# Kernel optimization log

Hardware: AMD Instinct MI355X
Metric: run time of the kernel (lower is better)

Reference implementation:

```python
import jax, jax.numpy as jnp
import numpy as np

N = 4096
DIM = 128      # dim_in
HID = 256      # mlp hidden_dim
K_IN = 8       # k for linear_k

def _knn_edges(dist, k):
    # dist: [n,n]; k nearest neighbors excluding self (matches heapq loop)
    n = dist.shape[0]
    d = jnp.where(jnp.eye(n, dtype=bool), jnp.inf, dist)
    nbr = jax.lax.top_k(-d, k)[1]                     # [n,k] indices of k smallest
    src = jnp.repeat(jnp.arange(n), k)                # res[0] = i
    dst = nbr.reshape(-1)                             # res[1] = neighbor
    return src, dst

def _gcn_conv(x, src, dst, W, b):
    # torch_geometric GCNConv: add self loops + symmetric normalization
    n = x.shape[0]
    loop = jnp.arange(n)
    s = jnp.concatenate([src, loop])
    t = jnp.concatenate([dst, loop])
    xw = x @ W
    deg = jax.ops.segment_sum(jnp.ones(s.shape[0], x.dtype), t, num_segments=n)
    dinv = jax.lax.rsqrt(deg)                         # deg >= 1 due to self loops
    norm = dinv[s] * dinv[t]
    out = jax.ops.segment_sum(norm[:, None] * xw[s], t, num_segments=n)
    return out + b

def _gcn(x, src, dst, Wg1, bg1, Wg2, bg2):
    h = jax.nn.relu(_gcn_conv(x, src, dst, Wg1, bg1))
    h = _gcn_conv(h, src, dst, Wg2, bg2)              # dropout is identity in eval
    return jax.nn.log_softmax(h, axis=1)

def _conv2d(x, w, b):
    y = jax.lax.conv_general_dilated(x, w, (1, 1), 'SAME',
        dimension_numbers=('NCHW', 'OIHW', 'NCHW'))
    return y + b.reshape(1, -1, 1, 1)

def setup_inputs():
    key = jax.random.key(0)
    ks = jax.random.split(key, 20)
    f32 = jnp.float32
    def w(k, shape):
        fan = shape[0]
        return (jax.random.uniform(k, shape, f32) * 2 - 1) * (1.0 / np.sqrt(fan))
    return {
        'data_x_1': jax.random.normal(ks[0], (1, N, 4), f32),
        'data_x_2': jax.random.normal(ks[1], (1, N, K_IN, 4), f32),
        'Wk': w(ks[2], (K_IN, 1)),        'bk': jnp.zeros((1,), f32),
        'Wg1': w(ks[3], (8, DIM // 2)),   'bg1': jnp.zeros((DIM // 2,), f32),
        'Wg2': w(ks[4], (DIM // 2, DIM)), 'bg2': jnp.zeros((DIM,), f32),
        'Wq': w(ks[5], (3 * DIM, DIM)),   'bq': jnp.zeros((DIM,), f32),
        'Wkey': w(ks[6], (3 * DIM, DIM)), 'bkey': jnp.zeros((DIM,), f32),
        'Woff': w(ks[7], (4, DIM)),       'boff': jnp.zeros((DIM,), f32),
        'pw': jnp.full((1,), 0.25, f32),
        'Wf1': w(ks[8], (DIM, HID)),      'bf1': jnp.zeros((HID,), f32),
        'Wf2': w(ks[9], (HID, HID)),      'bf2': jnp.zeros((HID,), f32),
        'Wf3': w(ks[10], (HID, 4)),       'bf3': jnp.zeros((4,), f32),
        'Wcy3': w(ks[11], (1, 1, 1, 3)),  'bcy3': jnp.zeros((1,), f32),
        'Wcx3': w(ks[12], (1, 1, 3, 1)),  'bcx3': jnp.zeros((1,), f32),
        'Wcy5': w(ks[13], (1, 1, 1, 5)),  'bcy5': jnp.zeros((1,), f32),
        'Wcx5': w(ks[14], (1, 1, 5, 1)),  'bcx5': jnp.zeros((1,), f32),
        'Wcy9': w(ks[15], (1, 1, 1, 9)),  'bcy9': jnp.zeros((1,), f32),
        'Wcx9': w(ks[16], (1, 1, 9, 1)),  'bcx9': jnp.zeros((1,), f32),
    }

def reference(data_x_1, data_x_2, Wk, bk, Wg1, bg1, Wg2, bg2, Wq, bq, Wkey, bkey,
              Woff, boff, pw, Wf1, bf1, Wf2, bf2, Wf3, bf3,
              Wcy3, bcy3, Wcx3, bcx3, Wcy5, bcy5, Wcx5, bcx5, Wcy9, bcy9, Wcx9, bcx9):
    # linear_k over k dimension: [1,n,k,4] -> transpose -> [1,n,4,k] -> [1,n,4]
    dx2 = jnp.swapaxes(data_x_2, 2, 3)
    dx2_out = (dx2 @ Wk + bk)[..., 0]
    data_x = jnp.concatenate([data_x_1, dx2_out], axis=2)   # [1,n,8]
    Ot = data_x[:, :, 4:]                                   # [1,n,4]

    pos = data_x[:, :, 0:2]
    diff = pos[:, :, None, :] - pos[:, None, :, :]          # [1,n,n,2]
    distances = jnp.linalg.norm(diff, axis=3)               # [1,n,n]
    maxd = jnp.max(distances, axis=2, keepdims=True)
    oushi_atte = 1.0 - distances / maxd                     # [1,n,n]

    x0 = data_x[0]
    dist0 = jax.lax.stop_gradient(distances[0])             # knn on detached dist
    embs = []
    for kk in (3, 5, 9):
        src, dst = _knn_edges(dist0, kk)
        embs.append(_gcn(x0, src, dst, Wg1, bg1, Wg2, bg2)[None])
    embedding = jnp.concatenate(embs, axis=2)               # [1,n,3*DIM]

    query = embedding @ Wq + bq                             # [1,n,DIM]
    key_t = embedding @ Wkey + bkey
    scores = jnp.einsum('bnd,bmd->bnm', query, key_t) / jnp.sqrt(jnp.float32(DIM))
    A = scores / jnp.max(scores, axis=2, keepdims=True)     # [1,n,n]

    A4 = A[None]                                            # [1,1,n,n]
    c3 = _conv2d(A4, Wcy3, bcy3) + _conv2d(A4, Wcx3, bcx3)
    c5 = _conv2d(A4, Wcy5, bcy5) + _conv2d(A4, Wcx5, bcx5)
    c9 = _conv2d(A4, Wcy9, bcy9) + _conv2d(A4, Wcx9, bcx9)

    A_cat = jnp.concatenate([A, oushi_atte, c3[0], c5[0], c9[0]], axis=2)  # [1,n,5n]
    A_cat = (A_cat - A_cat.min()) / (A_cat.max() - A_cat.min())

    Ot5 = jnp.tile(Ot, (1, 5, 1))                           # [1,5n,4]
    h = jnp.matmul(A_cat, Ot5)                              # [1,n,4]
    h = h @ Woff + boff                                     # [1,n,DIM]
    h = jnp.where(h > 0, h, pw * h)                         # PReLU (scalar weight)
    h = jax.nn.relu(h @ Wf1 + bf1)
    h = jax.nn.relu(h @ Wf2 + bf2)
    return h @ Wf3 + bf3                                    # [1,n,4]
```

## Files before the change

kernel.cpp:

```cpp
#include <hip/hip_runtime.h>
#include <math.h>

#define NN 4096

typedef __bf16 bf16x8 __attribute__((ext_vector_type(8)));
typedef float  f32x4  __attribute__((ext_vector_type(4)));

static __device__ __forceinline__ unsigned enc_f(float f){
    unsigned u = __float_as_uint(f);
    return (u & 0x80000000u) ? ~u : (u | 0x80000000u);
}
static __device__ __forceinline__ float dec_f(unsigned u){
    unsigned b = (u & 0x80000000u) ? (u & 0x7fffffffu) : ~u;
    return __uint_as_float(b);
}
static __device__ __forceinline__ float4 shfl4(float4 v, int src){
    float4 r;
    r.x = __shfl(v.x, src, 64);
    r.y = __shfl(v.y, src, 64);
    r.z = __shfl(v.z, src, 64);
    r.w = __shfl(v.w, src, 64);
    return r;
}

__global__ void k_prep(const float* __restrict__ dx1, const float* __restrict__ dx2,
                       const float* __restrict__ Wk, const float* __restrict__ bk,
                       float* __restrict__ x0, float* __restrict__ colsum){
    int n = blockIdx.x*blockDim.x + threadIdx.x;
    if (n >= NN) return;
    float wk[8];
    #pragma unroll
    for (int j=0;j<8;j++) wk[j] = Wk[j];
    float bkv = bk[0];
    #pragma unroll
    for (int c=0;c<4;c++) x0[n*8+c] = dx1[n*4+c];
    #pragma unroll
    for (int c=0;c<4;c++){
        float acc = bkv;
        #pragma unroll
        for (int j=0;j<8;j++) acc += dx2[(n*8+j)*4+c]*wk[j];
        x0[n*8+4+c] = acc;
        atomicAdd(&colsum[c], acc);
    }
}

__global__ void k_ty(const float* __restrict__ x0,
        const float* __restrict__ Wcy3, const float* __restrict__ Wcy5, const float* __restrict__ Wcy9,
        float* __restrict__ Ty){
    int j = blockIdx.x*256 + threadIdx.x;
    if (j >= NN) return;
    float Cy[9];
    #pragma unroll
    for (int o=-4;o<=4;o++){
        float c = Wcy9[o+4];
        if (o>=-2 && o<=2) c += Wcy5[o+2];
        if (o>=-1 && o<=1) c += Wcy3[o+1];
        Cy[o+4] = c;
    }
    float4 acc = {0,0,0,0};
    #pragma unroll
    for (int o=-4;o<=4;o++){
        int jj = j - o;
        if ((unsigned)jj < NN){
            float4 ot = *(const float4*)&x0[jj*8+4];
            float c = Cy[o+4];
            acc.x += c*ot.x; acc.y += c*ot.y; acc.z += c*ot.z; acc.w += c*ot.w;
        }
    }
    *(float4*)&Ty[j*4] = acc;
}

__global__ __launch_bounds__(256) void k_dist(const float* __restrict__ dx1,
        const float* __restrict__ x0,
        float* __restrict__ maxd, int* __restrict__ nbr,
        int* __restrict__ cnt3, int* __restrict__ cnt5, int* __restrict__ cnt9,
        float* __restrict__ dOt){
    __shared__ float2 ps[NN];
    int tid = threadIdx.x;
    for (int j=tid; j<NN; j+=256){
        float4 v = *(const float4*)&dx1[j*4];
        ps[j] = make_float2(v.x, v.y);
    }
    __syncthreads();
    int lane = tid & 63;
    int i = blockIdx.x*4 + (tid>>6);
    float2 pi = ps[i];
    unsigned long long best[9];
    #pragma unroll
    for (int q=0;q<9;q++) best[q] = ~0ULL;
    float lmax = 0.f;
    float4 dacc = {0,0,0,0};
    for (int t=0;t<64;t++){
        int j = (t<<6) | lane;
        float2 p = ps[j];
        float dx = pi.x - p.x, dy = pi.y - p.y;
        float d = sqrtf(dx*dx + dy*dy);
        lmax = fmaxf(lmax, d);
        float4 otj = *(const float4*)&x0[j*8+4];
        dacc.x += d*otj.x; dacc.y += d*otj.y; dacc.z += d*otj.z; dacc.w += d*otj.w;
        unsigned long long cand = ((unsigned long long)__float_as_uint(d) << 32) | (unsigned)j;
        if (j != i && cand < best[8]){
            best[8] = cand;
            #pragma unroll
            for (int q=8; q>0; --q){
                if (best[q] < best[q-1]){ unsigned long long tm=best[q]; best[q]=best[q-1]; best[q-1]=tm; }
            }
        }
    }
    #pragma unroll
    for (int m=1;m<64;m<<=1){
        lmax = fmaxf(lmax, __shfl_xor(lmax, m, 64));
        dacc.x += __shfl_xor(dacc.x, m, 64);
        dacc.y += __shfl_xor(dacc.y, m, 64);
        dacc.z += __shfl_xor(dacc.z, m, 64);
        dacc.w += __shfl_xor(dacc.w, m, 64);
    }
    if (lane==0){
        maxd[i] = lmax;
        *(float4*)&dOt[i*4] = dacc;
    }
    for (int t=0;t<9;t++){
        unsigned long long w = best[0];
        #pragma unroll
        for (int m=1;m<64;m<<=1){
            unsigned long long o = __shfl_xor(w, m, 64);
            if (o < w) w = o;
        }
        if (best[0] == w){
            #pragma unroll
            for (int q=0;q<8;q++) best[q] = best[q+1];
            best[8] = ~0ULL;
        }
        if (lane==0){
            int j = (int)(w & 0xffffffffu);
            nbr[i*9+t] = j;
            atomicAdd(&cnt9[j], 1);
            if (t<5) atomicAdd(&cnt5[j], 1);
            if (t<3) atomicAdd(&cnt3[j], 1);
        }
    }
}

__global__ __launch_bounds__(256) void k_scan(const int* __restrict__ cnt3,
        const int* __restrict__ cnt5, const int* __restrict__ cnt9,
        int* __restrict__ offc, float* __restrict__ dinvc){
    __shared__ int part[256];
    int tid = threadIdx.x;
    for (int g=0; g<3; g++){
        const int* cp = g==0?cnt3:(g==1?cnt5:cnt9);
        int base = tid*16;
        int loc[16]; int s=0;
        #pragma unroll
        for (int q=0;q<16;q++){ loc[q]=s; s += cp[base+q]; }
        part[tid]=s; __syncthreads();
        for (int d=1; d<256; d<<=1){
            int v = (tid>=d) ? part[tid-d] : 0;
            __syncthreads();
            part[tid] += v;
            __syncthreads();
        }
        int pre = (tid==0) ? 0 : part[tid-1];
        #pragma unroll
        for (int q=0;q<16;q++){
            offc[g*NN + base + q]  = pre + loc[q];
            dinvc[g*NN + base + q] = rsqrtf((float)cp[base+q] + 1.f);
        }
        __syncthreads();
    }
}

__global__ void k_fill(const int* __restrict__ nbr, const int* __restrict__ offc,
        int* __restrict__ cur, int* __restrict__ rev){
    int i = blockIdx.x*256 + threadIdx.x;
    if (i >= NN) return;
    #pragma unroll
    for (int t=0;t<9;t++){
        int j = nbr[i*9+t];
        int gmin = t<3 ? 0 : (t<5 ? 1 : 2);
        for (int g=gmin; g<3; g++){
            int pos = atomicAdd(&cur[g*NN+j], 1);
            int rb = (g==0) ? 0 : (g==1 ? NN*3 : NN*8);
            rev[rb + offc[g*NN+j] + pos] = i;
        }
    }
}

__global__ void k_y1(const float* __restrict__ x0, const float* __restrict__ Wg1,
                     float* __restrict__ xw){
    int idx = blockIdx.x*256 + threadIdx.x;
    if (idx >= NN*64) return;
    int n = idx>>6, c = idx&63;
    float acc = 0.f;
    #pragma unroll
    for (int k=0;k<8;k++) acc += x0[n*8+k]*Wg1[k*64+c];
    xw[idx] = acc;
}

__global__ __launch_bounds__(256) void k_h1y2(const float* __restrict__ xw,
        const int* __restrict__ offc,
        const int* __restrict__ cnt3, const int* __restrict__ cnt5, const int* __restrict__ cnt9,
        const int* __restrict__ rev, const float* __restrict__ dinvc,
        const float* __restrict__ bg1, const float* __restrict__ Wg2,
        float* __restrict__ y2){
    __shared__ float h1s[12][64];
    int n0 = blockIdx.x*4, tid = threadIdx.x;
    for (int s=tid; s<768; s+=256){
        int p = s>>6, k = s&63, g = p>>2, n = n0+(p&3);
        const int* cp = g==0?cnt3:(g==1?cnt5:cnt9);
        int rb = (g==0) ? 0 : (g==1 ? NN*3 : NN*8);
        int cnt = cp[n];
        int o = rb + offc[g*NN+n];
        float dv = dinvc[g*NN+n];
        float srow = dv*xw[n*64+k];
        for (int e=0;e<cnt;e++){
            int i = rev[o+e];
            srow += dinvc[g*NN+i]*xw[i*64+k];
        }
        float v = dv*srow + bg1[k];
        h1s[p][k] = v>0.f ? v : 0.f;
    }
    __syncthreads();
    int c = tid & 127, ph = tid>>7;
    float a6[6] = {0,0,0,0,0,0};
    for (int k=0;k<64;k++){
        float w = Wg2[k*128+c];
        #pragma unroll
        for (int q=0;q<6;q++) a6[q] += h1s[q*2+ph][k]*w;
    }
    #pragma unroll
    for (int q=0;q<6;q++){
        int p = q*2+ph, g = p>>2, n = n0+(p&3);
        float dv = dinvc[g*NN+n];
        y2[(size_t)g*NN*128 + (size_t)n*128 + c] = dv*a6[q];
    }
}

__global__ __launch_bounds__(128) void k_fin(const float* __restrict__ y2,
        const int* __restrict__ offc,
        const int* __restrict__ cnt3, const int* __restrict__ cnt5, const int* __restrict__ cnt9,
        const int* __restrict__ rev, const float* __restrict__ dinvc,
        const float* __restrict__ bg2, float* __restrict__ emb){
    __shared__ float sm[2], ss[2];
    int b = blockIdx.x;
    int n = b & (NN-1), g = b >> 12;
    const int* cp = g==0?cnt3:(g==1?cnt5:cnt9);
    int rb = (g==0) ? 0 : (g==1 ? NN*3 : NN*8);
    int cnt = cp[n];
    int o = rb + offc[g*NN+n];
    float dv = dinvc[g*NN+n];
    int c = threadIdx.x;
    const float* yg = y2 + (size_t)g*NN*128;
    float s = yg[(size_t)n*128 + c];
    for (int e=0;e<cnt;e++){
        int i = rev[o+e];
        s += yg[(size_t)i*128 + c];
    }
    float v = dv*s + bg2[c];
    float m = v;
    #pragma unroll
    for (int st=1;st<64;st<<=1) m = fmaxf(m, __shfl_xor(m, st, 64));
    if ((c&63)==0) sm[c>>6] = m;
    __syncthreads();
    m = fmaxf(sm[0], sm[1]);
    float e = expf(v - m);
    float t = e;
    #pragma unroll
    for (int st=1;st<64;st<<=1) t += __shfl_xor(t, st, 64);
    if ((c&63)==0) ss[c>>6] = t;
    __syncthreads();
    t = ss[0]+ss[1];
    emb[n*384 + g*128 + c] = v - m - logf(t);
}

__global__ __launch_bounds__(256) void k_qk(const float* __restrict__ emb,
        const float* __restrict__ Wq, const float* __restrict__ bq,
        const float* __restrict__ Wkey, const float* __restrict__ bkey,
        __bf16* __restrict__ qh, __bf16* __restrict__ ql,
        __bf16* __restrict__ kh, __bf16* __restrict__ kl){
    __shared__ float es[8][384];
    int n0 = blockIdx.x*8;
    int tid = threadIdx.x;
    for (int idx=tid; idx<8*384; idx+=256){
        int m = idx/384, k = idx%384;
        es[m][k] = emb[(n0+m)*384+k];
    }
    __syncthreads();
    int c = tid & 127;
    int sel = tid >> 7;
    const float* W = sel ? Wkey : Wq;
    float b = sel ? bkey[c] : bq[c];
    float acc[8];
    #pragma unroll
    for (int m=0;m<8;m++) acc[m]=b;
    for (int k=0;k<384;k++){
        float w = W[k*128+c];
        #pragma unroll
        for (int m=0;m<8;m++) acc[m] += es[m][k]*w;
    }
    __bf16* oh = sel ? kh : qh;
    __bf16* ol = sel ? kl : ql;
    #pragma unroll
    for (int m=0;m<8;m++){
        float v = acc[m];
        __bf16 h = (__bf16)v;
        oh[(size_t)(n0+m)*128+c] = h;
        ol[(size_t)(n0+m)*128+c] = (__bf16)(v - (float)h);
    }
}

__global__ __launch_bounds__(256) void k_scores(
        const __bf16* __restrict__ qh, const __bf16* __restrict__ ql,
        const __bf16* __restrict__ kh, const __bf16* __restrict__ kl,
        float* __restrict__ scores,
        unsigned* __restrict__ rowmaxenc, unsigned* __restrict__ rowminenc){
    int bx = blockIdx.x & 31;
    int by = blockIdx.x >> 5;
    int tid = threadIdx.x;
    int w = tid >> 6, lane = tid & 63;
    int li = lane & 15, g = lane >> 4;
    int r0 = by*128 + (w>>1)*64;
    int c0 = bx*128 + (w&1)*64;

    f32x4 acc[4][4] = {};
    for (int ks=0; ks<4; ++ks){
        int kofs = ks*32 + g*8;
        bf16x8 ah[4], al[4], bh[4], bl[4];
        #pragma unroll
        for (int f=0; f<4; ++f){
            ah[f] = *(const bf16x8*)&qh[(size_t)(r0+f*16+li)*128 + kofs];
            al[f] = *(const bf16x8*)&ql[(size_t)(r0+f*16+li)*128 + kofs];
            bh[f] = *(const bf16x8*)&kh[(size_t)(c0+f*16+li)*128 + kofs];
            bl[f] = *(const bf16x8*)&kl[(size_t)(c0+f*16+li)*128 + kofs];
        }
        #pragma unroll
        for (int fr=0; fr<4; ++fr){
            #pragma unroll
            for (int fc=0; fc<4; ++fc){
                acc[fr][fc] = __builtin_amdgcn_mfma_f32_16x16x32_bf16(ah[fr], bh[fc], acc[fr][fc], 0, 0, 0);
                acc[fr][fc] = __builtin_amdgcn_mfma_f32_16x16x32_bf16(ah[fr], bl[fc], acc[fr][fc], 0, 0, 0);
                acc[fr][fc] = __builtin_amdgcn_mfma_f32_16x16x32_bf16(al[fr], bh[fc], acc[fr][fc], 0, 0, 0);
            }
        }
    }
    #pragma unroll
    for (int fr=0; fr<4; ++fr){
        #pragma unroll
        for (int r=0; r<4; ++r){
            int row = r0 + fr*16 + g*4 + r;
            float mx = -INFINITY, mn = INFINITY;
            #pragma unroll
            for (int fc=0; fc<4; ++fc){
                float v = acc[fr][fc][r];
                scores[(size_t)row*NN + c0 + fc*16 + li] = v;
                mx = fmaxf(mx, v);
                mn = fminf(mn, v);
            }
            #pragma unroll
            for (int s=1; s<16; s<<=1){
                mx = fmaxf(mx, __shfl_xor(mx, s, 64));
                mn = fminf(mn, __shfl_xor(mn, s, 64));
            }
            if (li == 0){
                atomicMax(&rowmaxenc[row], enc_f(mx));
                atomicMin(&rowminenc[row], enc_f(mn));
            }
        }
    }
}

__global__ void k_invr(const unsigned* __restrict__ rowmaxenc, float* __restrict__ invr){
    int i = blockIdx.x*256 + threadIdx.x;
    if (i >= NN) return;
    invr[i] = 1.f/dec_f(rowmaxenc[i]);
}

__global__ __launch_bounds__(256) void k_cfuse(const float* __restrict__ scores,
        const float* __restrict__ invr,
        const float* __restrict__ x0, const float* __restrict__ Ty,
        const float* __restrict__ Wcy3, const float* __restrict__ Wcx3,
        const float* __restrict__ Wcy5, const float* __restrict__ Wcx5,
        const float* __restrict__ Wcy9, const float* __restrict__ Wcx9,
        const float* __restrict__ bcy3, const float* __restrict__ bcx3,
        const float* __restrict__ bcy5, const float* __restrict__ bcx5,
        const float* __restrict__ bcy9, const float* __restrict__ bcx9,
        float* __restrict__ mnmx, float* __restrict__ hpart){
    __shared__ float smn[4], smx[4];
    int tid = threadIdx.x;
    int w = tid >> 6, lane = tid & 63;
    int strip = blockIdx.x;
    int rb = blockIdx.y*4 + w;
    int i0 = rb*28;
    int colbase = strip*248 - 4 + lane*4;
    bool lv = (colbase >= 0) && (colbase + 3 < NN);
    bool outLane = (lane >= 1) && (lane < 63) && lv;

    float wy3[3],wx3[3],wy5[5],wx5[5],wy9[9],wx9[9];
    #pragma unroll
    for (int t=0;t<3;t++){ wy3[t]=Wcy3[t]; wx3[t]=Wcx3[t]; }
    #pragma unroll
    for (int t=0;t<5;t++){ wy5[t]=Wcy5[t]; wx5[t]=Wcx5[t]; }
    #pragma unroll
    for (int t=0;t<9;t++){ wy9[t]=Wcy9[t]; wx9[t]=Wcx9[t]; }
    float bc3 = bcy3[0]+bcx3[0];
    float bc5 = bcy5[0]+bcx5[0];
    float bc9 = bcy9[0]+bcx9[0];

    float4 ot[4], ty[4];
    #pragma unroll
    for (int c=0;c<4;c++){
        if (lv){
            ot[c] = *(const float4*)&x0[(colbase+c)*8+4];
            ty[c] = *(const float4*)&Ty[(colbase+c)*4];
        } else {
            ot[c] = make_float4(0,0,0,0);
            ty[c] = make_float4(0,0,0,0);
        }
    }

    float4 win[9];
    float mn = INFINITY, mx = -INFINITY;
    const int laneL = lane - 1, laneR = lane + 1;

    for (int tb = 0; tb < 4; ++tb){
        #pragma unroll
        for (int u = 0; u < 9; ++u){
            int t  = tb*9 + u;
            int ri = i0 - 4 + t;
            float4 a = make_float4(0,0,0,0);
            if (((unsigned)ri < NN) && lv){
                float iv = invr[ri];
                float4 v = *(const float4*)&scores[(size_t)ri*NN + colbase];
                a.x = v.x*iv; a.y = v.y*iv; a.z = v.z*iv; a.w = v.w*iv;
            }
            win[u] = a;
            int ro = i0 + t - 8;
            if (t >= 8 && ro < NN){
                float4 ctr = win[(u+5)%9];
                float4 wl = shfl4(ctr, laneL);
                float4 wr = shfl4(ctr, laneR);
                float cw[12] = {wl.x,wl.y,wl.z,wl.w, ctr.x,ctr.y,ctr.z,ctr.w, wr.x,wr.y,wr.z,wr.w};
                float4 pA = make_float4(0,0,0,0), pT = make_float4(0,0,0,0);
                if (outLane){
                    #pragma unroll
                    for (int c=0;c<4;c++){
                        float cx9 = ((win[(u+1)%9][c]*wx9[0] + win[(u+2)%9][c]*wx9[1]) + (win[(u+3)%9][c]*wx9[2] + win[(u+4)%9][c]*wx9[3]))
                                  + ((win[(u+5)%9][c]*wx9[4] + win[(u+6)%9][c]*wx9[5]) + (win[(u+7)%9][c]*wx9[6] + win[(u+8)%9][c]*wx9[7]))
                                  + win[u][c]*wx9[8];
                        float cx5 = ((win[(u+3)%9][c]*wx5[0] + win[(u+4)%9][c]*wx5[1]) + (win[(u+5)%9][c]*wx5[2] + win[(u+6)%9][c]*wx5[3]))
                                  + win[(u+7)%9][c]*wx5[4];
                        float cx3 = (win[(u+4)%9][c]*wx3[0] + win[(u+5)%9][c]*wx3[1]) + win[(u+6)%9][c]*wx3[2];
                        float cy9 = ((cw[c+0]*wy9[0] + cw[c+1]*wy9[1]) + (cw[c+2]*wy9[2] + cw[c+3]*wy9[3]))
                                  + ((cw[c+4]*wy9[4] + cw[c+5]*wy9[5]) + (cw[c+6]*wy9[6] + cw[c+7]*wy9[7]))
                                  + cw[c+8]*wy9[8];
                        float cy5 = ((cw[c+2]*wy5[0] + cw[c+3]*wy5[1]) + (cw[c+4]*wy5[2] + cw[c+5]*wy5[3]))
                                  + cw[c+6]*wy5[4];
                        float cy3 = (cw[c+3]*wy3[0] + cw[c+4]*wy3[1]) + cw[c+5]*wy3[2];
                        float c3v = cy3+cx3+bc3, c5v = cy5+cx5+bc5, c9v = cy9+cx9+bc9;
                        mn = fminf(mn, fminf(fminf(c3v,c5v),c9v));
                        mx = fmaxf(mx, fmaxf(fmaxf(c3v,c5v),c9v));
                        float av = cw[c+4];
                        pA.x += av*ot[c].x; pA.y += av*ot[c].y; pA.z += av*ot[c].z; pA.w += av*ot[c].w;
                        pT.x += av*ty[c].x; pT.y += av*ty[c].y; pT.z += av*ty[c].z; pT.w += av*ty[c].w;
                    }
                }
                #pragma unroll
                for (int m=1; m<64; m<<=1){
                    pA.x += __shfl_xor(pA.x, m, 64); pA.y += __shfl_xor(pA.y, m, 64);
                    pA.z += __shfl_xor(pA.z, m, 64); pA.w += __shfl_xor(pA.w, m, 64);
                    pT.x += __shfl_xor(pT.x, m, 64); pT.y += __shfl_xor(pT.y, m, 64);
                    pT.z += __shfl_xor(pT.z, m, 64); pT.w += __shfl_xor(pT.w, m, 64);
                }
                if (lane == 0){
                    float* hp = &hpart[((size_t)ro*17 + strip)*8];
                    *(float4*)hp = pA;
                    *(float4*)(hp+4) = pT;
                }
            }
        }
    }
    #pragma unroll
    for (int m=1; m<64; m<<=1){
        mn = fminf(mn, __shfl_xor(mn, m, 64));
        mx = fmaxf(mx, __shfl_xor(mx, m, 64));
    }
    if (lane == 0){ smn[w] = mn; smx[w] = mx; }
    __syncthreads();
    if (tid == 0){
        float a0 = fminf(fminf(smn[0],smn[1]), fminf(smn[2],smn[3]));
        float b0 = fmaxf(fmaxf(smx[0],smx[1]), fmaxf(smx[2],smx[3]));
        int bid = blockIdx.y*gridDim.x + blockIdx.x;
        mnmx[bid] = a0;
        mnmx[640 + bid] = b0;
    }
}

__global__ __launch_bounds__(256) void k_gmm(const float* __restrict__ mnmx,
        const unsigned* __restrict__ rowminenc, const unsigned* __restrict__ rowmaxenc,
        float* __restrict__ gmm){
    __shared__ float smn[256], smx[256];
    int tid = threadIdx.x;
    float mn = 0.f, mx = 1.f;
    for (int i=tid; i<NN; i+=256){
        float rmx = dec_f(rowmaxenc[i]);
        float q = dec_f(rowminenc[i]) / rmx;
        mn = fminf(mn, fminf(1.f, q));
        mx = fmaxf(mx, fmaxf(1.f, q));
    }
    for (int b=tid; b<629; b+=256){
        mn = fminf(mn, mnmx[b]);
        mx = fmaxf(mx, mnmx[640+b]);
    }
    smn[tid]=mn; smx[tid]=mx; __syncthreads();
    for (int s=128;s>0;s>>=1){
        if (tid<s){ smn[tid]=fminf(smn[tid],smn[tid+s]); smx[tid]=fmaxf(smx[tid],smx[tid+s]); }
        __syncthreads();
    }
    if (tid==0){ gmm[0]=smn[0]; gmm[1]=smx[0]; }
}

__global__ void k_hred(const float* __restrict__ hpart,
        const float* __restrict__ maxd, const float* __restrict__ dOt,
        const float* __restrict__ colsum,
        const float* __restrict__ bcy3, const float* __restrict__ bcx3,
        const float* __restrict__ bcy5, const float* __restrict__ bcx5,
        const float* __restrict__ bcy9, const float* __restrict__ bcx9,
        float* __restrict__ ASdot, float* __restrict__ Bv){
    int i = blockIdx.x*256 + threadIdx.x;
    if (i >= NN) return;
    float4 pa = {0,0,0,0}, pt = {0,0,0,0};
    const float* hp = &hpart[(size_t)i*17*8];
    #pragma unroll
    for (int s=0; s<17; ++s){
        float4 a = *(const float4*)&hp[s*8];
        float4 t = *(const float4*)&hp[s*8+4];
        pa.x+=a.x; pa.y+=a.y; pa.z+=a.z; pa.w+=a.w;
        pt.x+=t.x; pt.y+=t.y; pt.z+=t.z; pt.w+=t.w;
    }
    float imv = 1.f/maxd[i];
    float bcsum = bcy3[0]+bcx3[0]+bcy5[0]+bcx5[0]+bcy9[0]+bcx9[0];
    float k = 1.f + bcsum;
    float4 cs = *(const float4*)colsum;
    float4 dv = *(const float4*)&dOt[i*4];
    float4 b;
    b.x = cs.x*k - imv*dv.x + pt.x;
    b.y = cs.y*k - imv*dv.y + pt.y;
    b.z = cs.z*k - imv*dv.z + pt.z;
    b.w = cs.w*k - imv*dv.w + pt.w;
    *(float4*)&ASdot[i*4] = pa;
    *(float4*)&Bv[i*4]    = b;
}

__global__ void k_hfin(const float* __restrict__ ASdot, const float* __restrict__ Bv,
        const float* __restrict__ Wcx3, const float* __restrict__ Wcx5, const float* __restrict__ Wcx9,
        const float* __restrict__ gmm, const float* __restrict__ colsum,
        float* __restrict__ hfin){
    int i = blockIdx.x*256 + threadIdx.x;
    if (i >= NN) return;
    float Cx[9];
    #pragma unroll
    for (int o=-4;o<=4;o++){
        float c = Wcx9[o+4];
        if (o>=-2 && o<=2) c += Wcx5[o+2];
        if (o>=-1 && o<=1) c += Wcx3[o+1];
        Cx[o+4] = c;
    }
    float4 h = *(const float4*)&Bv[i*4];
    float4 a0 = *(const float4*)&ASdot[i*4];
    h.x += a0.x; h.y += a0.y; h.z += a0.z; h.w += a0.w;
    #pragma unroll
    for (int o=-4;o<=4;o++){
        int r = i + o;
        if ((unsigned)r < NN){
            float4 av = *(const float4*)&ASdot[r*4];
            float c = Cx[o+4];
            h.x += c*av.x; h.y += c*av.y; h.z += c*av.z; h.w += c*av.w;
        }
    }
    float mnv = gmm[0], mxv = gmm[1];
    float s = 1.f/(mxv-mnv), oa = -mnv*s;
    float4 cs = *(const float4*)colsum;
    float4 out;
    out.x = s*h.x + 5.f*oa*cs.x;
    out.y = s*h.y + 5.f*oa*cs.y;
    out.z = s*h.z + 5.f*oa*cs.z;
    out.w = s*h.w + 5.f*oa*cs.w;
    *(float4*)&hfin[i*4] = out;
}

__global__ __launch_bounds__(256) void k_mlp(const float* __restrict__ hfin,
        const float* __restrict__ Woff, const float* __restrict__ boff, const float* __restrict__ pw,
        const float* __restrict__ Wf1, const float* __restrict__ bf1,
        const float* __restrict__ Wf2, const float* __restrict__ bf2,
        const float* __restrict__ Wf3, const float* __restrict__ bf3,
        float* __restrict__ out){
    __shared__ float h1[8][128];
    __shared__ float h2[8][256];
    __shared__ float h3[8][256];
    __shared__ float4 red4[256];
    int n0 = blockIdx.x*8, tid = threadIdx.x;
    float p = pw[0];
    {
        int c = tid & 127, mb = (tid>>7)*4;
        #pragma unroll
        for (int mm=0; mm<4; mm++){
            int m = mb+mm;
            float v = boff[c];
            #pragma unroll
            for (int k=0;k<4;k++) v += hfin[(n0+m)*4+k]*Woff[k*128+c];
            h1[m][c] = v>0.f ? v : p*v;
        }
    }
    __syncthreads();
    {
        int c = tid;
        float acc[8];
        #pragma unroll
        for (int m=0;m<8;m++) acc[m] = bf1[c];
        for (int k=0;k<128;k++){
            float w = Wf1[k*256+c];
            #pragma unroll
            for (int m=0;m<8;m++) acc[m] += h1[m][k]*w;
        }
        #pragma unroll
        for (int m=0;m<8;m++) h2[m][c] = acc[m]>0.f?acc[m]:0.f;
    }
    __syncthreads();
    {
        int c = tid;
        float acc[8];
        #pragma unroll
        for (int m=0;m<8;m++) acc[m] = bf2[c];
        for (int k=0;k<256;k++){
            float w = Wf2[k*256+c];
            #pragma unroll
            for (int m=0;m<8;m++) acc[m] += h2[m][k]*w;
        }
        #pragma unroll
        for (int m=0;m<8;m++) h3[m][c] = acc[m]>0.f?acc[m]:0.f;
    }
    __syncthreads();
    float w3_0 = Wf3[tid*4+0], w3_1 = Wf3[tid*4+1], w3_2 = Wf3[tid*4+2], w3_3 = Wf3[tid*4+3];
    for (int m=0;m<8;m++){
        float hv = h3[m][tid];
        float4 r; r.x = hv*w3_0; r.y = hv*w3_1; r.z = hv*w3_2; r.w = hv*w3_3;
        red4[tid]=r; __syncthreads();
        for (int s=128;s>0;s>>=1){
            if(tid<s){
                red4[tid].x+=red4[tid+s].x; red4[tid].y+=red4[tid+s].y;
                red4[tid].z+=red4[tid+s].z; red4[tid].w+=red4[tid+s].w;
            }
            __syncthreads();
        }
        if (tid==0){
            float4 o;
            o.x = red4[0].x + bf3[0]; o.y = red4[0].y + bf3[1];
            o.z = red4[0].z + bf3[2]; o.w = red4[0].w + bf3[3];
            *(float4*)&out[(n0+m)*4] = o;
        }
        __syncthreads();
    }
}

extern "C" void kernel_launch(void* const* d_in, const int* in_sizes, int n_in,
                              void* d_out, int out_size, void* d_ws, size_t ws_size,
                              hipStream_t stream){
    const float* dx1  = (const float*)d_in[0];
    const float* dx2  = (const float*)d_in[1];
    const float* Wk   = (const float*)d_in[2];
    const float* bk   = (const float*)d_in[3];
    const float* Wg1  = (const float*)d_in[4];
    const float* bg1  = (const float*)d_in[5];
    const float* Wg2  = (const float*)d_in[6];
    const float* bg2  = (const float*)d_in[7];
    const float* Wq   = (const float*)d_in[8];
    const float* bq   = (const float*)d_in[9];
    const float* Wkey = (const float*)d_in[10];
    const float* bkey = (const float*)d_in[11];
    const float* Woff = (const float*)d_in[12];
    const float* boff = (const float*)d_in[13];
    const float* pw   = (const float*)d_in[14];
    const float* Wf1  = (const float*)d_in[15];
    const float* bf1  = (const float*)d_in[16];
    const float* Wf2  = (const float*)d_in[17];
    const float* bf2  = (const float*)d_in[18];
    const float* Wf3  = (const float*)d_in[19];
    const float* bf3  = (const float*)d_in[20];
    const float* Wcy3 = (const float*)d_in[21];
    const float* bcy3 = (const float*)d_in[22];
    const float* Wcx3 = (const float*)d_in[23];
    const float* bcx3 = (const float*)d_in[24];
    const float* Wcy5 = (const float*)d_in[25];
    const float* bcy5 = (const float*)d_in[26];
    const float* Wcx5 = (const float*)d_in[27];
    const float* bcx5 = (const float*)d_in[28];
    const float* Wcy9 = (const float*)d_in[29];
    const float* bcy9 = (const float*)d_in[30];
    const float* Wcx9 = (const float*)d_in[31];
    const float* bcx9 = (const float*)d_in[32];

    char* ws = (char*)d_ws;
    size_t off = 0;
    auto alloc = [&](size_t b)->void*{ void* p = ws + off; off += (b + 255) & ~(size_t)255; return p; };

    char* zbase = ws + off;
    float*    colsum    = (float*)   alloc(4*4);
    int*      cnt3      = (int*)     alloc((size_t)NN*4);
    int*      cnt5      = (int*)     alloc((size_t)NN*4);
    int*      cnt9      = (int*)     alloc((size_t)NN*4);
    int*      cur       = (int*)     alloc((size_t)3*NN*4);
    unsigned* rowmaxenc = (unsigned*)alloc((size_t)NN*4);
    size_t zbytes = (size_t)((ws + off) - zbase);
    unsigned* rowminenc = (unsigned*)alloc((size_t)NN*4);

    float* x0     = (float*)alloc((size_t)NN*8*4);
    float* maxd   = (float*)alloc((size_t)NN*4);
    int*   nbr    = (int*)  alloc((size_t)NN*9*4);
    int*   offc   = (int*)  alloc((size_t)3*NN*4);
    float* dinvc  = (float*)alloc((size_t)3*NN*4);
    int*   rev    = (int*)  alloc((size_t)NN*17*4);
    float* xw     = (float*)alloc((size_t)NN*64*4);
    float* y2     = (float*)alloc((size_t)3*NN*128*4);
    float* emb    = (float*)alloc((size_t)NN*384*4);
    __bf16* qh   = (__bf16*)alloc((size_t)NN*128*2);
    __bf16* ql   = (__bf16*)alloc((size_t)NN*128*2);
    __bf16* kh   = (__bf16*)alloc((size_t)NN*128*2);
    __bf16* kl   = (__bf16*)alloc((size_t)NN*128*2);
    float* scores = (float*)alloc((size_t)NN*NN*4);
    float* Tyb    = (float*)alloc((size_t)NN*4*4);
    float* invr   = (float*)alloc((size_t)NN*4);
    float* dOt    = (float*)alloc((size_t)NN*4*4);
    float* ASd    = (float*)alloc((size_t)NN*4*4);
    float* Bv     = (float*)alloc((size_t)NN*4*4);
    float* hpart  = (float*)alloc((size_t)NN*17*8*4);
    float* mnmx   = (float*)alloc((size_t)2*640*4);
    float* gmm    = (float*)alloc(2*4);
    float* hfin   = (float*)alloc((size_t)NN*4*4);
    (void)ws_size; (void)in_sizes; (void)n_in; (void)out_size;

    hipMemsetAsync(zbase, 0, zbytes, stream);
    hipMemsetAsync(rowminenc, 0xFF, (size_t)NN*4, stream);

    k_prep<<<16,256,0,stream>>>(dx1,dx2,Wk,bk,x0,colsum);
    k_ty  <<<16,256,0,stream>>>(x0,Wcy3,Wcy5,Wcy9,Tyb);
    k_dist<<<NN/4,256,0,stream>>>(dx1,x0,maxd,nbr,cnt3,cnt5,cnt9,dOt);
    k_scan<<<1,256,0,stream>>>(cnt3,cnt5,cnt9,offc,dinvc);
    k_fill<<<16,256,0,stream>>>(nbr,offc,cur,rev);

    k_y1  <<<NN*64/256,256,0,stream>>>(x0,Wg1,xw);
    k_h1y2<<<NN/4,256,0,stream>>>(xw,offc,cnt3,cnt5,cnt9,rev,dinvc,bg1,Wg2,y2);
    k_fin <<<NN*3,128,0,stream>>>(y2,offc,cnt3,cnt5,cnt9,rev,dinvc,bg2,emb);

    k_qk<<<NN/8,256,0,stream>>>(emb,Wq,bq,Wkey,bkey,qh,ql,kh,kl);
    k_scores<<<1024,256,0,stream>>>(qh,ql,kh,kl,scores,rowmaxenc,rowminenc);
    k_invr<<<16,256,0,stream>>>(rowmaxenc,invr);

    k_cfuse<<<dim3(17,37),256,0,stream>>>(scores,invr,x0,Tyb,
        Wcy3,Wcx3,Wcy5,Wcx5,Wcy9,Wcx9,
        bcy3,bcx3,bcy5,bcx5,bcy9,bcx9, mnmx, hpart);
    k_gmm<<<1,256,0,stream>>>(mnmx,rowminenc,rowmaxenc,gmm);
    k_hred<<<16,256,0,stream>>>(hpart,maxd,dOt,colsum,
        bcy3,bcx3,bcy5,bcx5,bcy9,bcx9, ASd, Bv);
    k_hfin<<<16,256,0,stream>>>(ASd,Bv,Wcx3,Wcx5,Wcx9,gmm,colsum,hfin);
    k_mlp<<<NN/8,256,0,stream>>>(hfin,Woff,boff,pw,Wf1,bf1,Wf2,bf2,Wf3,bf3,(float*)d_out);
}
```

Measured before the change: 334.5 us.

## Compute A·Ot and A·Ty via associativity q·(Kᵀ·Ot) instead of inside conv pass

```diff
diff --git a/kernel.cpp b/kernel.cpp
--- a/kernel.cpp
+++ b/kernel.cpp
@@ -374,22 +374,20 @@
     invr[i] = 1.f/dec_f(rowmaxenc[i]);
 }
 
-__global__ __launch_bounds__(256) void k_cfuse(const float* __restrict__ scores,
+__global__ __launch_bounds__(256) void k_cconv(const float* __restrict__ scores,
         const float* __restrict__ invr,
-        const float* __restrict__ x0, const float* __restrict__ Ty,
         const float* __restrict__ Wcy3, const float* __restrict__ Wcx3,
         const float* __restrict__ Wcy5, const float* __restrict__ Wcx5,
         const float* __restrict__ Wcy9, const float* __restrict__ Wcx9,
         const float* __restrict__ bcy3, const float* __restrict__ bcx3,
         const float* __restrict__ bcy5, const float* __restrict__ bcx5,
         const float* __restrict__ bcy9, const float* __restrict__ bcx9,
-        float* __restrict__ mnmx, float* __restrict__ hpart){
+        float* __restrict__ mnmx){
     __shared__ float smn[4], smx[4];
     int tid = threadIdx.x;
     int w = tid >> 6, lane = tid & 63;
     int strip = blockIdx.x;
-    int rb = blockIdx.y*4 + w;
-    int i0 = rb*28;
+    int i0 = (blockIdx.y*4 + w)*19;
     int colbase = strip*248 - 4 + lane*4;
     bool lv = (colbase >= 0) && (colbase + 3 < NN);
     bool outLane = (lane >= 1) && (lane < 63) && lv;
@@ -405,23 +403,11 @@
     float bc5 = bcy5[0]+bcx5[0];
     float bc9 = bcy9[0]+bcx9[0];
 
-    float4 ot[4], ty[4];
-    #pragma unroll
-    for (int c=0;c<4;c++){
-        if (lv){
-            ot[c] = *(const float4*)&x0[(colbase+c)*8+4];
-            ty[c] = *(const float4*)&Ty[(colbase+c)*4];
-        } else {
-            ot[c] = make_float4(0,0,0,0);
-            ty[c] = make_float4(0,0,0,0);
-        }
-    }
-
     float4 win[9];
     float mn = INFINITY, mx = -INFINITY;
     const int laneL = lane - 1, laneR = lane + 1;
 
-    for (int tb = 0; tb < 4; ++tb){
+    for (int tb = 0; tb < 3; ++tb){
         #pragma unroll
         for (int u = 0; u < 9; ++u){
             int t  = tb*9 + u;
@@ -438,9 +424,8 @@
                 float4 ctr = win[(u+5)%9];
                 float4 wl = shfl4(ctr, laneL);
                 float4 wr = shfl4(ctr, laneR);
-                float cw[12] = {wl.x,wl.y,wl.z,wl.w, ctr.x,ctr.y,ctr.z,ctr.w, wr.x,wr.y,wr.z,wr.w};
-                float4 pA = make_float4(0,0,0,0), pT = make_float4(0,0,0,0);
                 if (outLane){
+                    float cw[12] = {wl.x,wl.y,wl.z,wl.w, ctr.x,ctr.y,ctr.z,ctr.w, wr.x,wr.y,wr.z,wr.w};
                     #pragma unroll
                     for (int c=0;c<4;c++){
                         float cx9 = ((win[(u+1)%9][c]*wx9[0] + win[(u+2)%9][c]*wx9[1]) + (win[(u+3)%9][c]*wx9[2] + win[(u+4)%9][c]*wx9[3]))
@@ -458,22 +443,7 @@
                         float c3v = cy3+cx3+bc3, c5v = cy5+cx5+bc5, c9v = cy9+cx9+bc9;
                         mn = fminf(mn, fminf(fminf(c3v,c5v),c9v));
                         mx = fmaxf(mx, fmaxf(fmaxf(c3v,c5v),c9v));
-                        float av = cw[c+4];
-                        pA.x += av*ot[c].x; pA.y += av*ot[c].y; pA.z += av*ot[c].z; pA.w += av*ot[c].w;
-                        pT.x += av*ty[c].x; pT.y += av*ty[c].y; pT.z += av*ty[c].z; pT.w += av*ty[c].w;
                     }
-                }
-                #pragma unroll
-                for (int m=1; m<64; m<<=1){
-                    pA.x += __shfl_xor(pA.x, m, 64); pA.y += __shfl_xor(pA.y, m, 64);
-                    pA.z += __shfl_xor(pA.z, m, 64); pA.w += __shfl_xor(pA.w, m, 64);
-                    pT.x += __shfl_xor(pT.x, m, 64); pT.y += __shfl_xor(pT.y, m, 64);
-                    pT.z += __shfl_xor(pT.z, m, 64); pT.w += __shfl_xor(pT.w, m, 64);
-                }
-                if (lane == 0){
-                    float* hp = &hpart[((size_t)ro*17 + strip)*8];
-                    *(float4*)hp = pA;
-                    *(float4*)(hp+4) = pT;
                 }
             }
         }
@@ -490,7 +460,79 @@
         float b0 = fmaxf(fmaxf(smx[0],smx[1]), fmaxf(smx[2],smx[3]));
         int bid = blockIdx.y*gridDim.x + blockIdx.x;
         mnmx[bid] = a0;
-        mnmx[640 + bid] = b0;
+        mnmx[1024 + bid] = b0;
+    }
+}
+
+__global__ __launch_bounds__(256) void k_kot(const __bf16* __restrict__ kh, const __bf16* __restrict__ kl,
+        const float* __restrict__ x0, const float* __restrict__ Ty,
+        float* __restrict__ kOt){
+    __shared__ float red[256][8];
+    int d = blockIdx.x, tid = threadIdx.x;
+    float a[8] = {0,0,0,0,0,0,0,0};
+    for (int j = tid; j < NN; j += 256){
+        float kv = (float)kh[(size_t)j*128 + d] + (float)kl[(size_t)j*128 + d];
+        float4 ot = *(const float4*)&x0[j*8+4];
+        float4 ty = *(const float4*)&Ty[j*4];
+        a[0] += kv*ot.x; a[1] += kv*ot.y; a[2] += kv*ot.z; a[3] += kv*ot.w;
+        a[4] += kv*ty.x; a[5] += kv*ty.y; a[6] += kv*ty.z; a[7] += kv*ty.w;
+    }
+    #pragma unroll
+    for (int q=0;q<8;q++) red[tid][q] = a[q];
+    __syncthreads();
+    for (int s=128; s>0; s>>=1){
+        if (tid < s){
+            #pragma unroll
+            for (int q=0;q<8;q++) red[tid][q] += red[tid+s][q];
+        }
+        __syncthreads();
+    }
+    if (tid < 8) kOt[d*8 + tid] = red[0][tid];
+}
+
+__global__ __launch_bounds__(256) void k_asd(
+        const __bf16* __restrict__ qh, const __bf16* __restrict__ ql,
+        const float* __restrict__ kOt,
+        const unsigned* __restrict__ rowmaxenc, const float* __restrict__ maxd,
+        const float* __restrict__ dOt, const float* __restrict__ colsum,
+        const float* __restrict__ bcy3, const float* __restrict__ bcx3,
+        const float* __restrict__ bcy5, const float* __restrict__ bcx5,
+        const float* __restrict__ bcy9, const float* __restrict__ bcx9,
+        float* __restrict__ ASdot, float* __restrict__ Bv){
+    __shared__ float kst[128*8];
+    int tid = threadIdx.x;
+    for (int s = tid; s < 1024; s += 256) kst[s] = kOt[s];
+    __syncthreads();
+    int lane = tid & 63, r = tid >> 6;
+    int i = blockIdx.x*4 + r;
+    float a[8] = {0,0,0,0,0,0,0,0};
+    #pragma unroll
+    for (int dd=0; dd<2; ++dd){
+        int d = lane + dd*64;
+        float qv = (float)qh[(size_t)i*128 + d] + (float)ql[(size_t)i*128 + d];
+        #pragma unroll
+        for (int q=0;q<8;q++) a[q] += qv * kst[d*8+q];
+    }
+    #pragma unroll
+    for (int m=1; m<64; m<<=1){
+        #pragma unroll
+        for (int q=0;q<8;q++) a[q] += __shfl_xor(a[q], m, 64);
+    }
+    if (lane == 0){
+        float iv = 1.f/dec_f(rowmaxenc[i]);
+        float imv = 1.f/maxd[i];
+        float bcsum = bcy3[0]+bcx3[0]+bcy5[0]+bcx5[0]+bcy9[0]+bcx9[0];
+        float k = 1.f + bcsum;
+        float4 cs = *(const float4*)colsum;
+        float4 dv = *(const float4*)&dOt[i*4];
+        float4 pa = {iv*a[0], iv*a[1], iv*a[2], iv*a[3]};
+        float4 b;
+        b.x = cs.x*k - imv*dv.x + iv*a[4];
+        b.y = cs.y*k - imv*dv.y + iv*a[5];
+        b.z = cs.z*k - imv*dv.z + iv*a[6];
+        b.w = cs.w*k - imv*dv.w + iv*a[7];
+        *(float4*)&ASdot[i*4] = pa;
+        *(float4*)&Bv[i*4]    = b;
     }
 }
 
@@ -506,9 +548,9 @@
         mn = fminf(mn, fminf(1.f, q));
         mx = fmaxf(mx, fmaxf(1.f, q));
     }
-    for (int b=tid; b<629; b+=256){
+    for (int b=tid; b<918; b+=256){
         mn = fminf(mn, mnmx[b]);
-        mx = fmaxf(mx, mnmx[640+b]);
+        mx = fmaxf(mx, mnmx[1024+b]);
     }
     smn[tid]=mn; smx[tid]=mx; __syncthreads();
     for (int s=128;s>0;s>>=1){
@@ -516,38 +558,6 @@
         __syncthreads();
     }
     if (tid==0){ gmm[0]=smn[0]; gmm[1]=smx[0]; }
-}
-
-__global__ void k_hred(const float* __restrict__ hpart,
-        const float* __restrict__ maxd, const float* __restrict__ dOt,
-        const float* __restrict__ colsum,
-        const float* __restrict__ bcy3, const float* __restrict__ bcx3,
-        const float* __restrict__ bcy5, const float* __restrict__ bcx5,
-        const float* __restrict__ bcy9, const float* __restrict__ bcx9,
-        float* __restrict__ ASdot, float* __restrict__ Bv){
-    int i = blockIdx.x*256 + threadIdx.x;
-    if (i >= NN) return;
-    float4 pa = {0,0,0,0}, pt = {0,0,0,0};
-    const float* hp = &hpart[(size_t)i*17*8];
-    #pragma unroll
-    for (int s=0; s<17; ++s){
-        float4 a = *(const float4*)&hp[s*8];
-        float4 t = *(const float4*)&hp[s*8+4];
-        pa.x+=a.x; pa.y+=a.y; pa.z+=a.z; pa.w+=a.w;
-        pt.x+=t.x; pt.y+=t.y; pt.z+=t.z; pt.w+=t.w;
-    }
-    float imv = 1.f/maxd[i];
-    float bcsum = bcy3[0]+bcx3[0]+bcy5[0]+bcx5[0]+bcy9[0]+bcx9[0];
-    float k = 1.f + bcsum;
-    float4 cs = *(const float4*)colsum;
-    float4 dv = *(const float4*)&dOt[i*4];
-    float4 b;
-    b.x = cs.x*k - imv*dv.x + pt.x;
-    b.y = cs.y*k - imv*dv.y + pt.y;
-    b.z = cs.z*k - imv*dv.z + pt.z;
-    b.w = cs.w*k - imv*dv.w + pt.w;
-    *(float4*)&ASdot[i*4] = pa;
-    *(float4*)&Bv[i*4]    = b;
 }
 
 __global__ void k_hfin(const float* __restrict__ ASdot, const float* __restrict__ Bv,
@@ -729,10 +739,10 @@
     float* Tyb    = (float*)alloc((size_t)NN*4*4);
     float* invr   = (float*)alloc((size_t)NN*4);
     float* dOt    = (float*)alloc((size_t)NN*4*4);
+    float* kOt    = (float*)alloc((size_t)128*8*4);
     float* ASd    = (float*)alloc((size_t)NN*4*4);
     float* Bv     = (float*)alloc((size_t)NN*4*4);
-    float* hpart  = (float*)alloc((size_t)NN*17*8*4);
-    float* mnmx   = (float*)alloc((size_t)2*640*4);
+    float* mnmx   = (float*)alloc((size_t)2*1024*4);
     float* gmm    = (float*)alloc(2*4);
     float* hfin   = (float*)alloc((size_t)NN*4*4);
     (void)ws_size; (void)in_sizes; (void)n_in; (void)out_size;
@@ -753,13 +763,14 @@
     k_qk<<<NN/8,256,0,stream>>>(emb,Wq,bq,Wkey,bkey,qh,ql,kh,kl);
     k_scores<<<1024,256,0,stream>>>(qh,ql,kh,kl,scores,rowmaxenc,rowminenc);
     k_invr<<<16,256,0,stream>>>(rowmaxenc,invr);
-
-    k_cfuse<<<dim3(17,37),256,0,stream>>>(scores,invr,x0,Tyb,
+    k_kot<<<128,256,0,stream>>>(kh,kl,x0,Tyb,kOt);
+
+    k_cconv<<<dim3(17,54),256,0,stream>>>(scores,invr,
         Wcy3,Wcx3,Wcy5,Wcx5,Wcy9,Wcx9,
-        bcy3,bcx3,bcy5,bcx5,bcy9,bcx9, mnmx, hpart);
+        bcy3,bcx3,bcy5,bcx5,bcy9,bcx9, mnmx);
+    k_asd<<<NN/4,256,0,stream>>>(qh,ql,kOt,rowmaxenc,maxd,dOt,colsum,
+        bcy3,bcx3,bcy5,bcx5,bcy9,bcx9, ASd, Bv);
     k_gmm<<<1,256,0,stream>>>(mnmx,rowminenc,rowmaxenc,gmm);
-    k_hred<<<16,256,0,stream>>>(hpart,maxd,dOt,colsum,
-        bcy3,bcx3,bcy5,bcx5,bcy9,bcx9, ASd, Bv);
     k_hfin<<<16,256,0,stream>>>(ASd,Bv,Wcx3,Wcx5,Wcx9,gmm,colsum,hfin);
     k_mlp<<<NN/8,256,0,stream>>>(hfin,Woff,boff,pw,Wf1,bf1,Wf2,bf2,Wf3,bf3,(float*)d_out);
 }
```

Result: faster. 309.9 us (-7.4%).
